# Performance work log

Hardware: AMD Instinct MI355X
Metric: run time of the kernel (lower is better)

Reference implementation:

```python
import jax, jax.numpy as jnp
import numpy as np

SIGMA = 1.0


def _pairwise_max(q, fact_emb):
    # q: [B, N, D], fact_emb: [F, D]  (D = 3E)
    # Gaussian RBF kernel k(x,y) = exp(-||x-y||^2 / (2*sigma^2)), then max over F.
    q2 = jnp.sum(q * q, axis=-1, keepdims=True)            # [B, N, 1]
    f2 = jnp.sum(fact_emb * fact_emb, axis=-1)             # [F]
    qf = jnp.einsum('bnd,fd->bnf', q, fact_emb)            # [B, N, F]
    d2 = jnp.maximum(q2 + f2[None, None, :] - 2.0 * qf, 0.0)
    k = jnp.exp(-d2 / (2.0 * SIGMA ** 2))                  # [B, N, F]
    return jnp.max(k, axis=2)                              # [B, N]


def setup_inputs() -> dict:
    key = jax.random.key(0)
    ks = jax.random.split(key, 7)
    B, N, F, E = 8, 4000, 4000, 100
    return {
        'rel': jax.random.normal(ks[0], (B, E), jnp.float32),
        'arg1': jax.random.normal(ks[1], (B, E), jnp.float32),
        'arg2': jax.random.normal(ks[2], (B, E), jnp.float32),
        'fact_rel': jax.random.normal(ks[3], (F, E), jnp.float32),
        'fact_arg1': jax.random.normal(ks[4], (F, E), jnp.float32),
        'fact_arg2': jax.random.normal(ks[5], (F, E), jnp.float32),
        'entity_embeddings': jax.random.normal(ks[6], (N, E), jnp.float32),
    }


def reference(rel, arg1, arg2, fact_rel, fact_arg1, fact_arg2, entity_embeddings):
    B = rel.shape[0]
    N, E = entity_embeddings.shape
    fact_emb = jnp.concatenate([fact_rel, fact_arg1, fact_arg2], axis=1)  # [F, 3E]

    rel_b = jnp.broadcast_to(rel[:, None, :], (B, N, E))
    emb_b = jnp.broadcast_to(entity_embeddings[None, :, :], (B, N, E))

    # score_sp: query = [rel, arg1, entity]
    arg1_b = jnp.broadcast_to(arg1[:, None, :], (B, N, E))
    q_sp = jnp.concatenate([rel_b, arg1_b, emb_b], axis=2)  # [B, N, 3E]
    score_sp = _pairwise_max(q_sp, fact_emb)                # [B, N]

    # score_po: query = [rel, entity, arg2]
    arg2_b = jnp.broadcast_to(arg2[:, None, :], (B, N, E))
    q_po = jnp.concatenate([rel_b, emb_b, arg2_b], axis=2)  # [B, N, 3E]
    score_po = _pairwise_max(q_po, fact_emb)                # [B, N]

    return (score_sp, score_po)
```

## Files before the change

### kernel.cpp

```cpp
#include <hip/hip_runtime.h>
#include <math.h>

#define EDIM 100
#define KP   128
#define NF   4000
#define NN   4000
#define NB   8
#define NP   4096
#define BN   128
#define BF   64
#define FPB  4
#define NYB  16

#define CONVB (3 * NP * 16 / 256)
#define PREPB ((NP / 64) * NB)
#define E2B   ((NN + 255) / 256)

typedef __attribute__((ext_vector_type(8))) short short8;
typedef __attribute__((ext_vector_type(4))) float floatx4;

typedef const __attribute__((address_space(1))) unsigned int* gas_u32;
typedef __attribute__((address_space(3))) unsigned int* las_u32;

__device__ __align__(16) unsigned short g_A [NP * KP];
__device__ __align__(16) unsigned short g_B1[NP * KP];
__device__ __align__(16) unsigned short g_B2[NP * KP];
__device__ __align__(16) float g_P2[2 * 64 * 512];
__device__ float g_e2[NN];
__device__ float g_part[2 * NB * NYB * NP];

__device__ __forceinline__ unsigned short f2bf(float x) {
    union { float f; unsigned int u; } v; v.f = x;
    unsigned int r = v.u + 0x7FFFu + ((v.u >> 16) & 1u);
    return (unsigned short)(r >> 16);
}

__device__ __forceinline__ float row16_min(float x) {
    int i;
    i = __builtin_amdgcn_mov_dpp(__float_as_int(x), 0x140, 0xF, 0xF, false);
    x = fminf(x, __int_as_float(i));
    i = __builtin_amdgcn_mov_dpp(__float_as_int(x), 0x141, 0xF, 0xF, false);
    x = fminf(x, __int_as_float(i));
    i = __builtin_amdgcn_mov_dpp(__float_as_int(x), 0x1B, 0xF, 0xF, false);
    x = fminf(x, __int_as_float(i));
    i = __builtin_amdgcn_mov_dpp(__float_as_int(x), 0xB1, 0xF, 0xF, false);
    x = fminf(x, __int_as_float(i));
    return x;
}

__global__ void prep(const float* __restrict__ rel,  const float* __restrict__ arg1,
                     const float* __restrict__ arg2, const float* __restrict__ frel,
                     const float* __restrict__ fa1,  const float* __restrict__ fa2,
                     const float* __restrict__ ent) {
    const int bx = blockIdx.x;
    const int t  = threadIdx.x;

    if (bx < CONVB) {
        int plane = bx >> 8;
        int local = ((bx & 255) << 8) | t;
        int row = local >> 4, j = local & 15;
        const float* src = (plane == 0) ? ent : (plane == 1) ? fa1 : fa2;
        unsigned short* dst = (plane == 0) ? g_A : (plane == 1) ? g_B1 : g_B2;
        short8 o = (short8){0, 0, 0, 0, 0, 0, 0, 0};
        if (row < NF && j <= 12) {
            if (j < 12) {
                float4 v0 = *(const float4*)(src + row * EDIM + j * 8);
                float4 v1 = *(const float4*)(src + row * EDIM + j * 8 + 4);
                o[0] = (short)f2bf(v0.x); o[1] = (short)f2bf(v0.y);
                o[2] = (short)f2bf(v0.z); o[3] = (short)f2bf(v0.w);
                o[4] = (short)f2bf(v1.x); o[5] = (short)f2bf(v1.y);
                o[6] = (short)f2bf(v1.z); o[7] = (short)f2bf(v1.w);
            } else {
                float4 v0 = *(const float4*)(src + row * EDIM + 96);
                o[0] = (short)f2bf(v0.x); o[1] = (short)f2bf(v0.y);
                o[2] = (short)f2bf(v0.z); o[3] = (short)f2bf(v0.w);
            }
        }
        *(short8*)(dst + row * KP + j * 8) = o;
    } else if (bx < CONVB + PREPB) {
        int pb = bx - CONVB;
        int b   = pb >> 6;
        int fbx = pb & 63;
        int lane = t & 63;
        int wv = t >> 6;
        int fl = lane & 15;
        int kq = lane >> 4;
        int f = fbx * 64 + wv * 16 + fl;
        int fr = (f < NF) ? f : (NF - 1);

        float nf = 0.f, dr = 0.f, d1 = 0.f, d2 = 0.f, qr = 0.f, q1 = 0.f, q2 = 0.f;
        for (int i = 0; i < 25; i++) {
            int k = kq * 25 + i;
            float vr = frel[fr * EDIM + k];
            float v1 = fa1[fr * EDIM + k];
            float v2 = fa2[fr * EDIM + k];
            float rb = rel[b * EDIM + k];
            float a1 = arg1[b * EDIM + k];
            float a2 = arg2[b * EDIM + k];
            nf += vr * vr + v1 * v1 + v2 * v2;
            dr = fmaf(rb, vr, dr);
            d1 = fmaf(a1, v1, d1);
            d2 = fmaf(a2, v2, d2);
            qr = fmaf(rb, rb, qr);
            q1 = fmaf(a1, a1, q1);
            q2 = fmaf(a2, a2, q2);
        }
        nf += __shfl_xor(nf, 16); nf += __shfl_xor(nf, 32);
        dr += __shfl_xor(dr, 16); dr += __shfl_xor(dr, 32);
        d1 += __shfl_xor(d1, 16); d1 += __shfl_xor(d1, 32);
        d2 += __shfl_xor(d2, 16); d2 += __shfl_xor(d2, 32);
        qr += __shfl_xor(qr, 16); qr += __shfl_xor(qr, 32);
        q1 += __shfl_xor(q1, 16); q1 += __shfl_xor(q1, 32);
        q2 += __shfl_xor(q2, 16); q2 += __shfl_xor(q2, 32);
        if (kq == 0) {
            float psp = nf + qr + q1 - 2.f * (dr + d1);
            float ppo = nf + qr + q2 - 2.f * (dr + d2);
            if (f >= NF) { psp = __builtin_inff(); ppo = __builtin_inff(); }
            int fblk = f >> 6;
            int cc = f & 15;
            int ft = (f & 63) >> 4;
            int chunk = cc * 8 + (b ^ (cc & 7));
            g_P2[(0 * 64 + fblk) * 512 + chunk * 4 + ft] = psp;
            g_P2[(1 * 64 + fblk) * 512 + chunk * 4 + ft] = ppo;
        }
    } else {
        int n = (bx - CONVB - PREPB) * 256 + t;
        if (n < NN) {
            const float4* ep = (const float4*)(ent + n * EDIM);
            float s = 0.f;
            #pragma unroll
            for (int i = 0; i < EDIM / 4; i++) {
                float4 v = ep[i];
                s += v.x * v.x + v.y * v.y + v.z * v.z + v.w * v.w;
            }
            g_e2[n] = s;
        }
    }
}

__global__ void __launch_bounds__(256, 2) main_kernel() {
    __shared__ __align__(16) unsigned short sB[2][BF * 128];
    __shared__ __align__(16) float sP[2][512];

    const int t = threadIdx.x;
    const int n0 = blockIdx.x * BN;
    const int by = blockIdx.y;
    const int g  = blockIdx.z;
    const int lane = t & 63;
    const int c = lane & 15;
    const int q = lane >> 4;
    const int w = t >> 6;
    const int w32 = w * 32;

    const unsigned short* gB = g ? g_B1 : g_B2;

    short8 afrag[2][4];
    #pragma unroll
    for (int mt = 0; mt < 2; mt++)
        #pragma unroll
        for (int s = 0; s < 4; s++)
            afrag[mt][s] = *(const short8*)(g_A + (n0 + w32 + mt * 16 + c) * KP + (s * 4 + q) * 8);

    floatx4 m2[NB][2];
    #pragma unroll
    for (int b = 0; b < NB; b++)
        #pragma unroll
        for (int mt = 0; mt < 2; mt++)
            m2[b][mt] = (floatx4){__builtin_inff(), __builtin_inff(),
                                  __builtin_inff(), __builtin_inff()};

    auto stage = [&](int buf, int fb) {
        const int f0r = fb * BF;
        #pragma unroll
        for (int j = 0; j < 4; j++) {
            int ck = (w * 4 + j) * 64 + lane;
            int rw = ck >> 4, ch = ck & 15;
            int src = (f0r + rw) * 16 + (ch ^ (rw & 15));
            __builtin_amdgcn_global_load_lds(
                (gas_u32)(gB + src * 8),
                (las_u32)(&sB[buf][(w * 4 + j) * 512]),
                16, 0, 0);
        }
        if (w < 2)
            __builtin_amdgcn_global_load_lds(
                (gas_u32)(g_P2 + (g * 64 + fb) * 512 + w * 256 + lane * 4),
                (las_u32)(&sP[buf][w * 256]),
                16, 0, 0);
    };

    stage(0, by * FPB);
    __syncthreads();

    #pragma unroll 1
    for (int ib = 0; ib < FPB; ib++) {
        const int cur = ib & 1;
        if (ib + 1 < FPB) stage(cur ^ 1, by * FPB + ib + 1);

        const short8* pB = (const short8*)sB[cur];
        floatx4 acc[2][4];
        #pragma unroll
        for (int mt = 0; mt < 2; mt++)
            #pragma unroll
            for (int ft = 0; ft < 4; ft++)
                acc[mt][ft] = (floatx4){0.f, 0.f, 0.f, 0.f};

        #pragma unroll
        for (int s = 0; s < 4; s++) {
            const int base = s * 4 + q;
            #pragma unroll
            for (int ft = 0; ft < 4; ft++) {
                short8 bb = pB[(ft * 16 + c) * 16 + (base ^ c)];
                acc[0][ft] = __builtin_amdgcn_mfma_f32_16x16x32_bf16(afrag[0][s], bb, acc[0][ft], 0, 0, 0);
                acc[1][ft] = __builtin_amdgcn_mfma_f32_16x16x32_bf16(afrag[1][s], bb, acc[1][ft], 0, 0, 0);
            }
        }

        const float* Pf = sP[cur];
        #pragma unroll
        for (int b = 0; b < NB; b++) {
            floatx4 p = *(const floatx4*)(Pf + (c * 8 + (b ^ (c & 7))) * 4);
            #pragma unroll
            for (int mt = 0; mt < 2; mt++) {
                #pragma unroll
                for (int r = 0; r < 4; r++) {
                    float t0 = fmaf(-2.f, acc[mt][0][r], p[0]);
                    float t1 = fmaf(-2.f, acc[mt][1][r], p[1]);
                    float t2 = fmaf(-2.f, acc[mt][2][r], p[2]);
                    float t3 = fmaf(-2.f, acc[mt][3][r], p[3]);
                    float u = fminf(fminf(t0, t1), t2);
                    m2[b][mt][r] = fminf(fminf(u, t3), m2[b][mt][r]);
                }
            }
        }
        if (ib + 1 < FPB) __syncthreads();
    }

    #pragma unroll
    for (int b = 0; b < NB; b++)
        #pragma unroll
        for (int mt = 0; mt < 2; mt++)
            #pragma unroll
            for (int r = 0; r < 4; r++)
                m2[b][mt][r] = row16_min(m2[b][mt][r]);

    if (c == 0) {
        #pragma unroll
        for (int b = 0; b < NB; b++)
            #pragma unroll
            for (int mt = 0; mt < 2; mt++)
                *(float4*)&g_part[((g * NB + b) * NYB + by) * NP +
                                  n0 + w32 + mt * 16 + q * 4] =
                    (float4){m2[b][mt][0], m2[b][mt][1], m2[b][mt][2], m2[b][mt][3]};
    }
}

__global__ void finalize(float* __restrict__ out) {
    int idx = blockIdx.x * 256 + threadIdx.x;
    if (idx >= 2 * NB * NN) return;
    int sb = idx / NN;
    int n = idx % NN;
    float m = __builtin_inff();
    #pragma unroll
    for (int j = 0; j < NYB; j += 2) {
        float a = g_part[(sb * NYB + j) * NP + n];
        float b = g_part[(sb * NYB + j + 1) * NP + n];
        m = fminf(m, fminf(a, b));
    }
    float d2 = fmaxf(m + g_e2[n], 0.f);
    out[idx] = expf(-0.5f * d2);
}

extern "C" void kernel_launch(void* const* d_in, const int* in_sizes, int n_in,
                              void* d_out, int out_size, void* d_ws, size_t ws_size,
                              hipStream_t stream) {
    const float* rel  = (const float*)d_in[0];
    const float* arg1 = (const float*)d_in[1];
    const float* arg2 = (const float*)d_in[2];
    const float* frel = (const float*)d_in[3];
    const float* fa1  = (const float*)d_in[4];
    const float* fa2  = (const float*)d_in[5];
    const float* ent  = (const float*)d_in[6];
    float* out = (float*)d_out;

    prep<<<dim3(CONVB + PREPB + E2B), 256, 0, stream>>>(rel, arg1, arg2, frel, fa1, fa2, ent);
    main_kernel<<<dim3(NP / BN, NYB, 2), 256, 0, stream>>>();
    finalize<<<(2 * NB * NN + 255) / 256, 256, 0, stream>>>(out);
}
```

Baseline: 112.5 us.

## Read MFMA operands directly from global memory and restage prep through shared memory

The main kernel stops staging fact tiles and bias tables into LDS with async global-to-LDS loads and double buffering. It now reads B fragments and the P tables straight from global memory (relying on the cache), drops the block barriers and the XOR swizzle, and raises launch bounds to 3 blocks per CU. The prep kernel is reorganized so each block stages 64 fact rows in padded shared memory and computes all 8 batches, using 64 blocks instead of 512. The trade is losing explicit prefetch and overlap in exchange for higher occupancy and less synchronization.

```diff
diff --git a/kernel.cpp b/kernel.cpp
--- a/kernel.cpp
+++ b/kernel.cpp
@@ -13,14 +13,11 @@
 #define NYB  16
 
 #define CONVB (3 * NP * 16 / 256)
-#define PREPB ((NP / 64) * NB)
+#define PREPB 64
 #define E2B   ((NN + 255) / 256)
 
 typedef __attribute__((ext_vector_type(8))) short short8;
 typedef __attribute__((ext_vector_type(4))) float floatx4;
-
-typedef const __attribute__((address_space(1))) unsigned int* gas_u32;
-typedef __attribute__((address_space(3))) unsigned int* las_u32;
 
 __device__ __align__(16) unsigned short g_A [NP * KP];
 __device__ __align__(16) unsigned short g_B1[NP * KP];
@@ -52,6 +49,7 @@
                      const float* __restrict__ arg2, const float* __restrict__ frel,
                      const float* __restrict__ fa1,  const float* __restrict__ fa2,
                      const float* __restrict__ ent) {
+    __shared__ float sF[64 * 101];
     const int bx = blockIdx.x;
     const int t  = threadIdx.x;
 
@@ -78,50 +76,56 @@
         }
         *(short8*)(dst + row * KP + j * 8) = o;
     } else if (bx < CONVB + PREPB) {
-        int pb = bx - CONVB;
-        int b   = pb >> 6;
-        int fbx = pb & 63;
-        int lane = t & 63;
-        int wv = t >> 6;
-        int fl = lane & 15;
-        int kq = lane >> 4;
-        int f = fbx * 64 + wv * 16 + fl;
-        int fr = (f < NF) ? f : (NF - 1);
-
-        float nf = 0.f, dr = 0.f, d1 = 0.f, d2 = 0.f, qr = 0.f, q1 = 0.f, q2 = 0.f;
-        for (int i = 0; i < 25; i++) {
-            int k = kq * 25 + i;
-            float vr = frel[fr * EDIM + k];
-            float v1 = fa1[fr * EDIM + k];
-            float v2 = fa2[fr * EDIM + k];
-            float rb = rel[b * EDIM + k];
-            float a1 = arg1[b * EDIM + k];
-            float a2 = arg2[b * EDIM + k];
-            nf += vr * vr + v1 * v1 + v2 * v2;
-            dr = fmaf(rb, vr, dr);
-            d1 = fmaf(a1, v1, d1);
-            d2 = fmaf(a2, v2, d2);
-            qr = fmaf(rb, rb, qr);
-            q1 = fmaf(a1, a1, q1);
-            q2 = fmaf(a2, a2, q2);
-        }
-        nf += __shfl_xor(nf, 16); nf += __shfl_xor(nf, 32);
-        dr += __shfl_xor(dr, 16); dr += __shfl_xor(dr, 32);
-        d1 += __shfl_xor(d1, 16); d1 += __shfl_xor(d1, 32);
-        d2 += __shfl_xor(d2, 16); d2 += __shfl_xor(d2, 32);
-        qr += __shfl_xor(qr, 16); qr += __shfl_xor(qr, 32);
-        q1 += __shfl_xor(q1, 16); q1 += __shfl_xor(q1, 32);
-        q2 += __shfl_xor(q2, 16); q2 += __shfl_xor(q2, 32);
-        if (kq == 0) {
-            float psp = nf + qr + q1 - 2.f * (dr + d1);
-            float ppo = nf + qr + q2 - 2.f * (dr + d2);
+        const int fbx = bx - CONVB;
+        const int fl = t & 63;
+        const int bq = t >> 6;
+        const int f  = fbx * 64 + fl;
+
+        float nf = 0.f;
+        float dr[2], d1[2], d2[2], qr[2], q1n[2], q2n[2];
+
+        #pragma unroll 3
+        for (int pass = 0; pass < 3; pass++) {
+            const float* src = (pass == 0) ? frel : (pass == 1) ? fa1 : fa2;
+            const float* qv  = (pass == 0) ? rel  : (pass == 1) ? arg1 : arg2;
+            __syncthreads();
+            #pragma unroll
+            for (int i = 0; i < 25; i++) {
+                int idx = i * 256 + t;
+                int row = idx / 100, col = idx - row * 100;
+                int fr = fbx * 64 + row; if (fr > NF - 1) fr = NF - 1;
+                sF[row * 101 + col] = src[fr * EDIM + col];
+            }
+            __syncthreads();
+            float dot0 = 0.f, dot1 = 0.f, qn0 = 0.f, qn1 = 0.f, fn = 0.f;
+            #pragma unroll 4
+            for (int k = 0; k < EDIM; k++) {
+                float fv = sF[fl * 101 + k];
+                float u0 = qv[bq * EDIM + k];
+                float u1 = qv[(bq + 4) * EDIM + k];
+                dot0 = fmaf(fv, u0, dot0);
+                dot1 = fmaf(fv, u1, dot1);
+                qn0  = fmaf(u0, u0, qn0);
+                qn1  = fmaf(u1, u1, qn1);
+                fn   = fmaf(fv, fv, fn);
+            }
+            nf += fn;
+            if (pass == 0) { dr[0] = dot0; dr[1] = dot1; qr[0] = qn0; qr[1] = qn1; }
+            else if (pass == 1) { d1[0] = dot0; d1[1] = dot1; q1n[0] = qn0; q1n[1] = qn1; }
+            else { d2[0] = dot0; d2[1] = dot1; q2n[0] = qn0; q2n[1] = qn1; }
+        }
+
+        const int cc = fl & 15;
+        const int ft = fl >> 4;
+        #pragma unroll
+        for (int bi = 0; bi < 2; bi++) {
+            int b = bq + bi * 4;
+            float psp = nf + qr[bi] + q1n[bi] - 2.f * (dr[bi] + d1[bi]);
+            float ppo = nf + qr[bi] + q2n[bi] - 2.f * (dr[bi] + d2[bi]);
             if (f >= NF) { psp = __builtin_inff(); ppo = __builtin_inff(); }
-            int fblk = f >> 6;
-            int cc = f & 15;
-            int ft = (f & 63) >> 4;
-            int chunk = cc * 8 + (b ^ (cc & 7));
-            g_P2[(0 * 64 + fblk) * 512 + chunk * 4 + ft] = psp;
-            g_P2[(1 * 64 + fblk) * 512 + chunk * 4 + ft] = ppo;
+            int chunk = cc * 8 + b;
+            g_P2[(0 * 64 + fbx) * 512 + chunk * 4 + ft] = psp;
+            g_P2[(1 * 64 + fbx) * 512 + chunk * 4 + ft] = ppo;
         }
     } else {
         int n = (bx - CONVB - PREPB) * 256 + t;
@@ -138,10 +142,7 @@
     }
 }
 
-__global__ void __launch_bounds__(256, 2) main_kernel() {
-    __shared__ __align__(16) unsigned short sB[2][BF * 128];
-    __shared__ __align__(16) float sP[2][512];
-
+__global__ void __launch_bounds__(256, 3) main_kernel() {
     const int t = threadIdx.x;
     const int n0 = blockIdx.x * BN;
     const int by = blockIdx.y;
@@ -169,34 +170,11 @@
             m2[b][mt] = (floatx4){__builtin_inff(), __builtin_inff(),
                                   __builtin_inff(), __builtin_inff()};
 
-    auto stage = [&](int buf, int fb) {
-        const int f0r = fb * BF;
-        #pragma unroll
-        for (int j = 0; j < 4; j++) {
-            int ck = (w * 4 + j) * 64 + lane;
-            int rw = ck >> 4, ch = ck & 15;
-            int src = (f0r + rw) * 16 + (ch ^ (rw & 15));
-            __builtin_amdgcn_global_load_lds(
-                (gas_u32)(gB + src * 8),
-                (las_u32)(&sB[buf][(w * 4 + j) * 512]),
-                16, 0, 0);
-        }
-        if (w < 2)
-            __builtin_amdgcn_global_load_lds(
-                (gas_u32)(g_P2 + (g * 64 + fb) * 512 + w * 256 + lane * 4),
-                (las_u32)(&sP[buf][w * 256]),
-                16, 0, 0);
-    };
-
-    stage(0, by * FPB);
-    __syncthreads();
-
     #pragma unroll 1
     for (int ib = 0; ib < FPB; ib++) {
-        const int cur = ib & 1;
-        if (ib + 1 < FPB) stage(cur ^ 1, by * FPB + ib + 1);
-
-        const short8* pB = (const short8*)sB[cur];
+        const int fb = by * FPB + ib;
+        const int f0 = fb * BF;
+
         floatx4 acc[2][4];
         #pragma unroll
         for (int mt = 0; mt < 2; mt++)
@@ -206,19 +184,18 @@
 
         #pragma unroll
         for (int s = 0; s < 4; s++) {
-            const int base = s * 4 + q;
             #pragma unroll
             for (int ft = 0; ft < 4; ft++) {
-                short8 bb = pB[(ft * 16 + c) * 16 + (base ^ c)];
+                short8 bb = *(const short8*)(gB + (f0 + ft * 16 + c) * KP + (s * 4 + q) * 8);
                 acc[0][ft] = __builtin_amdgcn_mfma_f32_16x16x32_bf16(afrag[0][s], bb, acc[0][ft], 0, 0, 0);
                 acc[1][ft] = __builtin_amdgcn_mfma_f32_16x16x32_bf16(afrag[1][s], bb, acc[1][ft], 0, 0, 0);
             }
         }
 
-        const float* Pf = sP[cur];
+        const float* Pf = g_P2 + (g * 64 + fb) * 512;
         #pragma unroll
         for (int b = 0; b < NB; b++) {
-            floatx4 p = *(const floatx4*)(Pf + (c * 8 + (b ^ (c & 7))) * 4);
+            floatx4 p = *(const floatx4*)(Pf + (c * 8 + b) * 4);
             #pragma unroll
             for (int mt = 0; mt < 2; mt++) {
                 #pragma unroll
@@ -232,7 +209,6 @@
                 }
             }
         }
-        if (ib + 1 < FPB) __syncthreads();
     }
 
     #pragma unroll
```

New measurement: 147.4 us. 31.0% more time.
